# Performance work log

Measured on AMD Instinct MI355X. Metric: run time of the kernel, lower is better.

Reference implementation:

```python
import jax, jax.numpy as jnp
import numpy as np

CUTOFF = 0.32178
SCALE = 2.0 * 28.0 * CUTOFF


def setup_inputs() -> dict:
    rng = np.random.default_rng(0)
    N, E0, K = 20000, 160000, 9
    pos_np = rng.uniform(0.0, 28.0, (N, 2)).astype(np.float32)
    s = rng.integers(0, N, E0)
    d = rng.integers(0, N, E0)
    keep = s != d
    ei = np.stack([s[keep], d[keep]])
    ei = np.concatenate([ei, ei[::-1]], axis=1)
    ei = np.unique(ei.T, axis=0).T.astype(np.int64)  # symmetric, deduped, no self-loops

    def ncut(ei_, pos_):
        r, c = ei_
        w = np.linalg.norm(pos_[r] - pos_[c], axis=1)
        deg = np.bincount(r, minlength=pos_.shape[0]).astype(np.float64)
        deg[deg == 0] = 1.0
        return w * (1.0 / deg[r] + 1.0 / deg[c])

    def graclus(ei_, w, n):
        # greedy heavy-weight matching in node-index order (graclus-style)
        o = np.argsort(ei_[0], kind='stable')
        r, c, ww = ei_[0][o], ei_[1][o], w[o]
        ptr = np.searchsorted(r, np.arange(n + 1))
        cl = -np.ones(n, dtype=np.int64)
        cid = 0
        for i in range(n):
            if cl[i] >= 0:
                continue
            best, bw = -1, -1.0
            for k in range(ptr[i], ptr[i + 1]):
                j = c[k]
                if cl[j] < 0 and j != i and ww[k] > bw:
                    bw, best = ww[k], j
            cl[i] = cid
            if best >= 0:
                cl[best] = cid
            cid += 1
        return cl, cid

    def pool_edges(ei_, cl):
        m = cl[ei_]
        m = m[:, m[0] != m[1]]
        return np.unique(m.T, axis=0).T

    def seg_mean(v, cl, c):
        out = np.zeros((c, v.shape[1]), dtype=np.float64)
        np.add.at(out, cl, v)
        cnt = np.bincount(cl, minlength=c).astype(np.float64)
        return (out / cnt[:, None]).astype(np.float32)

    cl1, C1 = graclus(ei, ncut(ei, pos_np), N)
    ei2 = pool_edges(ei, cl1)
    pos2 = seg_mean(pos_np, cl1, C1)
    cl2, C2 = graclus(ei2, ncut(ei2, pos2), C1)
    ei3 = pool_edges(ei2, cl2)

    def prm(*shape):
        return jnp.asarray(rng.normal(0.0, 0.1, shape).astype(np.float32))

    def sig(k):
        return jnp.asarray(rng.uniform(0.5, 1.5, (k, 2)).astype(np.float32))

    return {
        'x': jnp.asarray(rng.standard_normal((N, 1)).astype(np.float32)),
        'pos': jnp.asarray(pos_np),
        'edge_index1': jnp.asarray(ei, dtype=jnp.int32),
        'cluster1': jnp.asarray(cl1, dtype=jnp.int32),
        'edge_index2': jnp.asarray(ei2, dtype=jnp.int32),
        'cluster2': jnp.asarray(cl2, dtype=jnp.int32),
        'edge_index3': jnp.asarray(ei3, dtype=jnp.int32),
        'batch': jnp.zeros((C2,), dtype=jnp.int32),
        'g1': prm(1, K, 32), 'mu1': prm(K, 2) + 0.5, 'sigma1': sig(K), 'root1': prm(1, 32), 'b1': prm(32),
        'g2': prm(32, K, 64), 'mu2': prm(K, 2) + 0.5, 'sigma2': sig(K), 'root2': prm(32, 64), 'b2': prm(64),
        'g3': prm(64, K, 64), 'mu3': prm(K, 2) + 0.5, 'sigma3': sig(K), 'root3': prm(64, 64), 'b3': prm(64),
        'fw': prm(64, 128), 'fb': prm(128),
    }


def _pseudo(pos, ei):
    # edge pseudo-coordinates: (pos[col]-pos[row]) / (2*28*cutoff) + 0.5
    return (pos[ei[1]] - pos[ei[0]]) / SCALE + 0.5


def _gmm_conv(x, ei, ea, g, mu, sigma, root, bias, n):
    # GMMConv: mean over neighbors of sum_k gauss_k(e_ij) * (x_j @ G_k), plus root weight and bias
    row, col = ei[0], ei[1]
    d = ea[:, None, :] - mu[None]                                       # [E,K,2]
    w = jnp.exp(-0.5 * jnp.sum(d * d / (sigma[None] ** 2), axis=-1))    # [E,K]
    msg = jnp.einsum('ei,iko,ek->eo', x[row], g, w)                     # [E,out]
    agg = jax.ops.segment_sum(msg, col, num_segments=n)
    cnt = jax.ops.segment_sum(jnp.ones_like(col, dtype=x.dtype), col, num_segments=n)
    return agg / jnp.maximum(cnt, 1.0)[:, None] + x @ root + bias


def _seg_mean(v, seg, n):
    s = jax.ops.segment_sum(v, seg, num_segments=n)
    c = jax.ops.segment_sum(jnp.ones((v.shape[0],), v.dtype), seg, num_segments=n)
    return s / jnp.maximum(c, 1.0)[:, None]


def _forward(x, pos, edge_index1, cluster1, edge_index2, cluster2, edge_index3, batch,
             g1, mu1, sigma1, root1, b1, g2, mu2, sigma2, root2, b2,
             g3, mu3, sigma3, root3, b3, fw, fb):
    N = x.shape[0]
    C1 = cluster2.shape[0]
    C2 = batch.shape[0]
    h = jax.nn.elu(_gmm_conv(x, edge_index1, _pseudo(pos, edge_index1), g1, mu1, sigma1, root1, b1, N))
    h = jax.ops.segment_max(h, cluster1, num_segments=C1)               # max_pool x
    pos2 = _seg_mean(pos, cluster1, C1)                                  # max_pool pos (mean)
    h = jax.nn.elu(_gmm_conv(h, edge_index2, _pseudo(pos2, edge_index2), g2, mu2, sigma2, root2, b2, C1))
    h = jax.ops.segment_max(h, cluster2, num_segments=C2)
    pos3 = _seg_mean(pos2, cluster2, C2)
    h = jax.nn.elu(_gmm_conv(h, edge_index3, _pseudo(pos3, edge_index3), g3, mu3, sigma3, root3, b3, C2))
    gm = _seg_mean(h, batch, 1)                                          # global_mean_pool (1 graph)
    return gm @ fw + fb                                                  # forward returns fc1(x)


def reference(x, pos, edge_index1, cluster1, edge_index2, cluster2, edge_index3, batch,
              g1, mu1, sigma1, root1, b1, g2, mu2, sigma2, root2, b2,
              g3, mu3, sigma3, root3, b3, fw, fb):
    return _forward(x, pos, edge_index1, cluster1, edge_index2, cluster2, edge_index3, batch,
                    g1, mu1, sigma1, root1, b1, g2, mu2, sigma2, root2, b2,
                    g3, mu3, sigma3, root3, b3, fw, fb)
```

## Files before the change

kernel.cpp:

```cpp
#include <hip/hip_runtime.h>
#include <math.h>

static constexpr float SCALE_F = (float)(2.0 * 28.0 * 0.32178);

__device__ __forceinline__ unsigned mapf(float f){
    unsigned u = __float_as_uint(f);
    return (u & 0x80000000u) ? ~u : (u | 0x80000000u);
}
__device__ __forceinline__ float unmapf(unsigned m){
    unsigned u = (m & 0x80000000u) ? (m ^ 0x80000000u) : ~m;
    return __uint_as_float(u);
}
__device__ __forceinline__ float eluf(float x){ return x > 0.f ? x : expm1f(x); }

__global__ void init_all(unsigned* __restrict__ hmax, int nmax, float* __restrict__ zreg, int nz){
    int i = blockIdx.x*blockDim.x + threadIdx.x;
    int s = gridDim.x*blockDim.x;
    for (int k = i; k < nmax; k += s) hmax[k] = 0x007FFFFFu;
    for (int k = i; k < nz;   k += s) zreg[k] = 0.f;
}

__global__ void build_rowptr_all(const int* __restrict__ r1, int E1, int N1, int* __restrict__ rp1,
                                 const int* __restrict__ r2, int E2, int N2, int* __restrict__ rp2,
                                 const int* __restrict__ r3, int E3, int N3, int* __restrict__ rp3){
    int i = blockIdx.x*blockDim.x + threadIdx.x;
    const int* rows; int E; int n; int* rp;
    if (i <= N1)               { rows=r1; E=E1; n=i;            rp=rp1+n; }
    else if (i <= N1+1+N2)     { rows=r2; E=E2; n=i-(N1+1);     rp=rp2+n; }
    else if (i <= N1+N2+2+N3)  { rows=r3; E=E3; n=i-(N1+N2+2);  rp=rp3+n; }
    else return;
    int lo = 0, hi = E;
    while (lo < hi){ int mid = (lo+hi) >> 1; if (rows[mid] < n) lo = mid+1; else hi = mid; }
    *rp = lo;
}

__global__ __launch_bounds__(256) void l1_kernel(const float* __restrict__ x, const float* __restrict__ pos,
    const int* __restrict__ ei1, int E1, const int* __restrict__ rp1, const int* __restrict__ cl1,
    const float* __restrict__ g1, const float* __restrict__ mu1, const float* __restrict__ sg1,
    const float* __restrict__ rt1, const float* __restrict__ b1,
    unsigned* __restrict__ h2m, float* __restrict__ pos2s, float* __restrict__ cntc1, int N)
{
    int wv = threadIdx.x >> 6, lane = threadIdx.x & 63;
    int n = blockIdx.x*4 + wv;
    if (n >= N) return;
    const int* cols = ei1 + E1;
    float mx[9], my[9], ivx[9], ivy[9];
    #pragma unroll
    for (int k = 0; k < 9; k++){
        mx[k] = mu1[2*k]; my[k] = mu1[2*k+1];
        float sx = sg1[2*k], sy = sg1[2*k+1];
        ivx[k] = 1.f/(sx*sx); ivy[k] = 1.f/(sy*sy);
    }
    float px = pos[2*n], py = pos[2*n+1];
    int e0 = rp1[n], e1 = rp1[n+1];
    float s[9] = {0.f,0.f,0.f,0.f,0.f,0.f,0.f,0.f,0.f};
    for (int e = e0 + lane; e < e1; e += 64){
        int j = cols[e];
        float ux = (px - pos[2*j])/SCALE_F + 0.5f;
        float uy = (py - pos[2*j+1])/SCALE_F + 0.5f;
        float xj = x[j];
        #pragma unroll
        for (int k = 0; k < 9; k++){
            float dx = ux - mx[k], dy = uy - my[k];
            s[k] += xj * expf(-0.5f*(dx*dx*ivx[k] + dy*dy*ivy[k]));
        }
    }
    #pragma unroll
    for (int off = 32; off > 0; off >>= 1){
        #pragma unroll
        for (int k = 0; k < 9; k++) s[k] += __shfl_xor(s[k], off, 64);
    }
    float inv = 1.f / (float)max(e1 - e0, 1);
    int c = cl1[n];
    if (lane < 32){
        int o = lane;
        float acc = 0.f;
        #pragma unroll
        for (int k = 0; k < 9; k++) acc += g1[k*32+o] * s[k];
        float v = acc*inv + x[n]*rt1[o] + b1[o];
        atomicMax(&h2m[(size_t)c*32 + o], mapf(eluf(v)));
    }
    if (lane == 0){
        atomicAdd(&pos2s[2*c],   px);
        atomicAdd(&pos2s[2*c+1], py);
        atomicAdd(&cntc1[c], 1.f);
    }
}

__global__ __launch_bounds__(256) void l2_kernel(const unsigned* __restrict__ h2m,
    const float* __restrict__ pos2s, const float* __restrict__ cntc1,
    const int* __restrict__ ei2, int E2, const int* __restrict__ rp2, const int* __restrict__ cl2,
    const float* __restrict__ g2, const float* __restrict__ mu2, const float* __restrict__ sg2,
    const float* __restrict__ rt2, const float* __restrict__ b2,
    unsigned* __restrict__ h3m, float* __restrict__ pos3s, float* __restrict__ cntc2)
{
    int n = blockIdx.x, t = threadIdx.x;
    __shared__ float mus[18], ivs[18];
    __shared__ int   jc[64];
    __shared__ float Wc[64*9];
    __shared__ float Sp[8*288];
    __shared__ float Ssum[288];
    __shared__ float xn_s[32];
    __shared__ float red1[4*64], red2[4*64];
    if (t < 9){
        mus[2*t] = mu2[2*t]; mus[2*t+1] = mu2[2*t+1];
        float sx = sg2[2*t], sy = sg2[2*t+1];
        ivs[2*t] = 1.f/(sx*sx); ivs[2*t+1] = 1.f/(sy*sy);
    }
    if (t < 32) xn_s[t] = unmapf(h2m[(size_t)n*32 + t]);
    int e0 = rp2[n], e1 = rp2[n+1], deg = e1 - e0;
    float cn = fmaxf(cntc1[n], 1.f);
    float px = pos2s[2*n]/cn, py = pos2s[2*n+1]/cn;
    const int* cols = ei2 + E2;
    int i = t & 31, g = t >> 5;
    float sacc[9] = {0.f,0.f,0.f,0.f,0.f,0.f,0.f,0.f,0.f};
    __syncthreads();
    for (int base = e0; base < e1; base += 64){
        int ne = min(64, e1 - base);
        if (t < ne){
            int j = cols[base + t];
            jc[t] = j;
            float cj = fmaxf(cntc1[j], 1.f);
            float ux = (px - pos2s[2*j]/cj)/SCALE_F + 0.5f;
            float uy = (py - pos2s[2*j+1]/cj)/SCALE_F + 0.5f;
            #pragma unroll
            for (int k = 0; k < 9; k++){
                float dx = ux - mus[2*k], dy = uy - mus[2*k+1];
                Wc[t*9+k] = expf(-0.5f*(dx*dx*ivs[2*k] + dy*dy*ivs[2*k+1]));
            }
        }
        __syncthreads();
        for (int jj = g; jj < ne; jj += 8){
            int j = jc[jj];
            float xji = unmapf(h2m[(size_t)j*32 + i]);
            #pragma unroll
            for (int k = 0; k < 9; k++) sacc[k] += xji * Wc[jj*9 + k];
        }
        __syncthreads();
    }
    #pragma unroll
    for (int k = 0; k < 9; k++) Sp[g*288 + i*9 + k] = sacc[k];
    __syncthreads();
    for (int idx = t; idx < 288; idx += 256){
        float v = 0.f;
        #pragma unroll
        for (int gg = 0; gg < 8; gg++) v += Sp[gg*288 + idx];
        Ssum[idx] = v;
    }
    __syncthreads();
    int o = t & 63, p = t >> 6;
    float acc = 0.f;
    for (int idx = p*72; idx < p*72 + 72; idx++) acc += g2[idx*64 + o] * Ssum[idx];
    float racc = 0.f;
    #pragma unroll
    for (int ii = p*8; ii < p*8 + 8; ii++) racc += xn_s[ii] * rt2[ii*64 + o];
    red1[p*64+o] = acc; red2[p*64+o] = racc;
    __syncthreads();
    if (t < 64){
        float agg = red1[t] + red1[64+t] + red1[128+t] + red1[192+t];
        float rr  = red2[t] + red2[64+t] + red2[128+t] + red2[192+t];
        float inv = 1.f / (float)max(deg, 1);
        float h = eluf(agg*inv + rr + b2[t]);
        int c = cl2[n];
        atomicMax(&h3m[(size_t)c*64 + t], mapf(h));
        if (t == 0){
            atomicAdd(&pos3s[2*c],   px);
            atomicAdd(&pos3s[2*c+1], py);
            atomicAdd(&cntc2[c], 1.f);
        }
    }
}

__global__ __launch_bounds__(256) void l3_kernel(const unsigned* __restrict__ h3m,
    const float* __restrict__ pos3s, const float* __restrict__ cntc2,
    const int* __restrict__ ei3, int E3, const int* __restrict__ rp3,
    const float* __restrict__ g3, const float* __restrict__ mu3, const float* __restrict__ sg3,
    const float* __restrict__ rt3, const float* __restrict__ b3,
    float* __restrict__ gpart)
{
    int n = blockIdx.x, t = threadIdx.x;
    __shared__ float mus[18], ivs[18];
    __shared__ int   jc[64];
    __shared__ float Wc[64*9];
    __shared__ float Sp[4*576];
    __shared__ float Ssum[576];
    __shared__ float xn_s[64];
    __shared__ float red1[4*64], red2[4*64];
    if (t < 9){
        mus[2*t] = mu3[2*t]; mus[2*t+1] = mu3[2*t+1];
        float sx = sg3[2*t], sy = sg3[2*t+1];
        ivs[2*t] = 1.f/(sx*sx); ivs[2*t+1] = 1.f/(sy*sy);
    }
    if (t < 64) xn_s[t] = unmapf(h3m[(size_t)n*64 + t]);
    int e0 = rp3[n], e1 = rp3[n+1], deg = e1 - e0;
    float cn = fmaxf(cntc2[n], 1.f);
    float px = pos3s[2*n]/cn, py = pos3s[2*n+1]/cn;
    const int* cols = ei3 + E3;
    int i = t & 63, wv = t >> 6;
    float sacc[9] = {0.f,0.f,0.f,0.f,0.f,0.f,0.f,0.f,0.f};
    __syncthreads();
    for (int base = e0; base < e1; base += 64){
        int ne = min(64, e1 - base);
        if (t < ne){
            int j = cols[base + t];
            jc[t] = j;
            float cj = fmaxf(cntc2[j], 1.f);
            float ux = (px - pos3s[2*j]/cj)/SCALE_F + 0.5f;
            float uy = (py - pos3s[2*j+1]/cj)/SCALE_F + 0.5f;
            #pragma unroll
            for (int k = 0; k < 9; k++){
                float dx = ux - mus[2*k], dy = uy - mus[2*k+1];
                Wc[t*9+k] = expf(-0.5f*(dx*dx*ivs[2*k] + dy*dy*ivs[2*k+1]));
            }
        }
        __syncthreads();
        for (int jj = wv; jj < ne; jj += 4){
            int j = jc[jj];
            float xji = unmapf(h3m[(size_t)j*64 + i]);
            #pragma unroll
            for (int k = 0; k < 9; k++) sacc[k] += xji * Wc[jj*9 + k];
        }
        __syncthreads();
    }
    #pragma unroll
    for (int k = 0; k < 9; k++) Sp[wv*576 + i*9 + k] = sacc[k];
    __syncthreads();
    for (int idx = t; idx < 576; idx += 256){
        float v = Sp[idx] + Sp[576 + idx] + Sp[1152 + idx] + Sp[1728 + idx];
        Ssum[idx] = v;
    }
    __syncthreads();
    int o = t & 63, p = t >> 6;
    float acc = 0.f;
    for (int idx = p*144; idx < p*144 + 144; idx++) acc += g3[idx*64 + o] * Ssum[idx];
    float racc = 0.f;
    #pragma unroll
    for (int ii = p*16; ii < p*16 + 16; ii++) racc += xn_s[ii] * rt3[ii*64 + o];
    red1[p*64+o] = acc; red2[p*64+o] = racc;
    __syncthreads();
    if (t < 64){
        float agg = red1[t] + red1[64+t] + red1[128+t] + red1[192+t];
        float rr  = red2[t] + red2[64+t] + red2[128+t] + red2[192+t];
        float inv = 1.f / (float)max(deg, 1);
        float h = eluf(agg*inv + rr + b3[t]);
        atomicAdd(&gpart[(size_t)(n & 63)*64 + t], h);
    }
}

__global__ void final_kernel(const float* __restrict__ gpart, const float* __restrict__ fw,
                             const float* __restrict__ fb, float* __restrict__ out, int C2){
    __shared__ float gs[64];
    __shared__ float red[2*64];
    int t = threadIdx.x;
    int o = t & 63, h = t >> 6;
    float a = 0.f;
    for (int p = h*32; p < h*32 + 32; p++) a += gpart[p*64 + o];
    red[h*64 + o] = a;
    __syncthreads();
    if (t < 64) gs[t] = (red[t] + red[64+t]) / (float)C2;
    __syncthreads();
    float acc = fb[t];
    for (int o2 = 0; o2 < 64; o2++) acc += gs[o2] * fw[o2*128 + t];
    out[t] = acc;
}

extern "C" void kernel_launch(void* const* d_in, const int* in_sizes, int n_in,
                              void* d_out, int out_size, void* d_ws, size_t ws_size,
                              hipStream_t stream)
{
    const float* x    = (const float*)d_in[0];
    const float* pos  = (const float*)d_in[1];
    const int*   ei1  = (const int*)d_in[2];
    const int*   cl1  = (const int*)d_in[3];
    const int*   ei2  = (const int*)d_in[4];
    const int*   cl2  = (const int*)d_in[5];
    const int*   ei3  = (const int*)d_in[6];
    const float* g1   = (const float*)d_in[8];
    const float* mu1  = (const float*)d_in[9];
    const float* sg1  = (const float*)d_in[10];
    const float* rt1  = (const float*)d_in[11];
    const float* b1   = (const float*)d_in[12];
    const float* g2   = (const float*)d_in[13];
    const float* mu2  = (const float*)d_in[14];
    const float* sg2  = (const float*)d_in[15];
    const float* rt2  = (const float*)d_in[16];
    const float* b2   = (const float*)d_in[17];
    const float* g3   = (const float*)d_in[18];
    const float* mu3  = (const float*)d_in[19];
    const float* sg3  = (const float*)d_in[20];
    const float* rt3  = (const float*)d_in[21];
    const float* b3   = (const float*)d_in[22];
    const float* fw   = (const float*)d_in[23];
    const float* fb   = (const float*)d_in[24];
    float* out = (float*)d_out;

    const int N  = in_sizes[0];
    const int E1 = in_sizes[2] / 2;
    const int C1 = in_sizes[5];
    const int E2 = in_sizes[4] / 2;
    const int C2 = in_sizes[7];
    const int E3 = in_sizes[6] / 2;

    float* w = (float*)d_ws;
    size_t off = 0;
    int* rp1 = (int*)(w + off); off += (size_t)N + 1;
    int* rp2 = (int*)(w + off); off += (size_t)C1 + 1;
    int* rp3 = (int*)(w + off); off += (size_t)C2 + 1;
    unsigned* h2m = (unsigned*)(w + off); off += (size_t)C1 * 32;
    unsigned* h3m = (unsigned*)(w + off); off += (size_t)C2 * 64;
    float* pos2s = w + off; off += (size_t)2 * C1;
    float* cntc1 = w + off; off += (size_t)C1;
    float* pos3s = w + off; off += (size_t)2 * C2;
    float* cntc2 = w + off; off += (size_t)C2;
    float* gpart = w + off; off += 64*64;

    const int nmax = C1*32 + C2*64;
    const int nz   = 3*C1 + 3*C2 + 64*64;
    init_all<<<dim3(256), dim3(256), 0, stream>>>(h2m, nmax, pos2s, nz);

    int nrp = N + C1 + C2 + 3;
    build_rowptr_all<<<dim3((nrp + 255)/256), dim3(256), 0, stream>>>(
        ei1, E1, N, rp1, ei2, E2, C1, rp2, ei3, E3, C2, rp3);

    l1_kernel<<<dim3((N + 3)/4), dim3(256), 0, stream>>>(x, pos, ei1, E1, rp1, cl1,
        g1, mu1, sg1, rt1, b1, h2m, pos2s, cntc1, N);
    l2_kernel<<<dim3(C1), dim3(256), 0, stream>>>(h2m, pos2s, cntc1, ei2, E2, rp2, cl2,
        g2, mu2, sg2, rt2, b2, h3m, pos3s, cntc2);
    l3_kernel<<<dim3(C2), dim3(256), 0, stream>>>(h3m, pos3s, cntc2, ei3, E3, rp3,
        g3, mu3, sg3, rt3, b3, gpart);
    final_kernel<<<dim3(1), dim3(128), 0, stream>>>(gpart, fw, fb, out, C2);
}
```

Baseline: 246.1 us.

## Remap GMM conv layers to wave-per-node and merge prep kernels

```diff
diff --git a/kernel.cpp b/kernel.cpp
--- a/kernel.cpp
+++ b/kernel.cpp
@@ -13,35 +13,45 @@
 }
 __device__ __forceinline__ float eluf(float x){ return x > 0.f ? x : expm1f(x); }
 
-__global__ void init_all(unsigned* __restrict__ hmax, int nmax, float* __restrict__ zreg, int nz){
-    int i = blockIdx.x*blockDim.x + threadIdx.x;
-    int s = gridDim.x*blockDim.x;
-    for (int k = i; k < nmax; k += s) hmax[k] = 0x007FFFFFu;
-    for (int k = i; k < nz;   k += s) zreg[k] = 0.f;
-}
-
-__global__ void build_rowptr_all(const int* __restrict__ r1, int E1, int N1, int* __restrict__ rp1,
-                                 const int* __restrict__ r2, int E2, int N2, int* __restrict__ rp2,
-                                 const int* __restrict__ r3, int E3, int N3, int* __restrict__ rp3){
-    int i = blockIdx.x*blockDim.x + threadIdx.x;
-    const int* rows; int E; int n; int* rp;
-    if (i <= N1)               { rows=r1; E=E1; n=i;            rp=rp1+n; }
-    else if (i <= N1+1+N2)     { rows=r2; E=E2; n=i-(N1+1);     rp=rp2+n; }
-    else if (i <= N1+N2+2+N3)  { rows=r3; E=E3; n=i-(N1+N2+2);  rp=rp3+n; }
-    else return;
-    int lo = 0, hi = E;
-    while (lo < hi){ int mid = (lo+hi) >> 1; if (rows[mid] < n) lo = mid+1; else hi = mid; }
-    *rp = lo;
-}
-
-__global__ __launch_bounds__(256) void l1_kernel(const float* __restrict__ x, const float* __restrict__ pos,
+__device__ __forceinline__ void wave_sync(){
+    __builtin_amdgcn_wave_barrier();
+    asm volatile("s_waitcnt lgkmcnt(0)" ::: "memory");
+    __builtin_amdgcn_wave_barrier();
+}
+
+__global__ void prep_kernel(const float* __restrict__ x, const float* __restrict__ pos, int N,
+    const int* __restrict__ ei1, int E1, const int* __restrict__ ei2, int E2, int C1,
+    const int* __restrict__ ei3, int E3, int C2,
+    int* __restrict__ rp1, int* __restrict__ rp2, int* __restrict__ rp3,
+    unsigned* __restrict__ hmax, int nmax, float* __restrict__ zreg, int nz,
+    float4* __restrict__ xp1)
+{
+    int i0 = blockIdx.x*blockDim.x + threadIdx.x, gs = gridDim.x*blockDim.x;
+    for (int i = i0; i < nmax; i += gs) hmax[i] = 0x007FFFFFu;
+    for (int i = i0; i < nz;   i += gs) zreg[i] = 0.f;
+    for (int i = i0; i < N;    i += gs) xp1[i] = make_float4(pos[2*i], pos[2*i+1], x[i], 0.f);
+    int nrp = N + C1 + C2 + 3;
+    for (int i = i0; i < nrp; i += gs){
+        const int* rows; int E, n; int* rp;
+        if (i <= N)            { rows = ei1; E = E1; n = i;            rp = rp1 + n; }
+        else if (i <= N+1+C1)  { rows = ei2; E = E2; n = i - (N+1);    rp = rp2 + n; }
+        else                   { rows = ei3; E = E3; n = i - (N+C1+2); rp = rp3 + n; }
+        int lo = 0, hi = E;
+        while (lo < hi){ int m = (lo+hi) >> 1; if (rows[m] < n) lo = m+1; else hi = m; }
+        *rp = lo;
+    }
+}
+
+__global__ __launch_bounds__(256) void l1_kernel(const float4* __restrict__ xp1,
     const int* __restrict__ ei1, int E1, const int* __restrict__ rp1, const int* __restrict__ cl1,
     const float* __restrict__ g1, const float* __restrict__ mu1, const float* __restrict__ sg1,
     const float* __restrict__ rt1, const float* __restrict__ b1,
-    unsigned* __restrict__ h2m, float* __restrict__ pos2s, float* __restrict__ cntc1, int N)
-{
-    int wv = threadIdx.x >> 6, lane = threadIdx.x & 63;
-    int n = blockIdx.x*4 + wv;
+    unsigned* __restrict__ h2m, float4* __restrict__ pos2s4, int N)
+{
+    int t = threadIdx.x;
+    int lane = t & 63, wv = t >> 6;
+    int q = lane >> 4, il = lane & 15;
+    int n = (blockIdx.x*4 + wv)*4 + q;
     if (n >= N) return;
     const int* cols = ei1 + E1;
     float mx[9], my[9], ivx[9], ivy[9];
@@ -51,200 +61,183 @@
         float sx = sg1[2*k], sy = sg1[2*k+1];
         ivx[k] = 1.f/(sx*sx); ivy[k] = 1.f/(sy*sy);
     }
-    float px = pos[2*n], py = pos[2*n+1];
+    float4 me = xp1[n];
+    float px = me.x, py = me.y, xn = me.z;
     int e0 = rp1[n], e1 = rp1[n+1];
     float s[9] = {0.f,0.f,0.f,0.f,0.f,0.f,0.f,0.f,0.f};
-    for (int e = e0 + lane; e < e1; e += 64){
+    for (int e = e0 + il; e < e1; e += 16){
         int j = cols[e];
-        float ux = (px - pos[2*j])/SCALE_F + 0.5f;
-        float uy = (py - pos[2*j+1])/SCALE_F + 0.5f;
-        float xj = x[j];
+        float4 pj = xp1[j];
+        float ux = (px - pj.x)/SCALE_F + 0.5f;
+        float uy = (py - pj.y)/SCALE_F + 0.5f;
         #pragma unroll
         for (int k = 0; k < 9; k++){
             float dx = ux - mx[k], dy = uy - my[k];
-            s[k] += xj * expf(-0.5f*(dx*dx*ivx[k] + dy*dy*ivy[k]));
-        }
-    }
-    #pragma unroll
-    for (int off = 32; off > 0; off >>= 1){
+            s[k] += pj.z * expf(-0.5f*(dx*dx*ivx[k] + dy*dy*ivy[k]));
+        }
+    }
+    #pragma unroll
+    for (int off = 8; off > 0; off >>= 1){
         #pragma unroll
-        for (int k = 0; k < 9; k++) s[k] += __shfl_xor(s[k], off, 64);
+        for (int k = 0; k < 9; k++) s[k] += __shfl_xor(s[k], off, 16);
     }
     float inv = 1.f / (float)max(e1 - e0, 1);
     int c = cl1[n];
-    if (lane < 32){
-        int o = lane;
+    #pragma unroll
+    for (int oo = 0; oo < 2; oo++){
+        int o = il + oo*16;
         float acc = 0.f;
         #pragma unroll
         for (int k = 0; k < 9; k++) acc += g1[k*32+o] * s[k];
-        float v = acc*inv + x[n]*rt1[o] + b1[o];
+        float v = acc*inv + xn*rt1[o] + b1[o];
         atomicMax(&h2m[(size_t)c*32 + o], mapf(eluf(v)));
     }
-    if (lane == 0){
-        atomicAdd(&pos2s[2*c],   px);
-        atomicAdd(&pos2s[2*c+1], py);
-        atomicAdd(&cntc1[c], 1.f);
+    if (il == 0){
+        atomicAdd(&pos2s4[c].x, px);
+        atomicAdd(&pos2s4[c].y, py);
+        atomicAdd(&pos2s4[c].z, 1.f);
     }
 }
 
 __global__ __launch_bounds__(256) void l2_kernel(const unsigned* __restrict__ h2m,
-    const float* __restrict__ pos2s, const float* __restrict__ cntc1,
+    const float4* __restrict__ pos2s4,
     const int* __restrict__ ei2, int E2, const int* __restrict__ rp2, const int* __restrict__ cl2,
     const float* __restrict__ g2, const float* __restrict__ mu2, const float* __restrict__ sg2,
     const float* __restrict__ rt2, const float* __restrict__ b2,
-    unsigned* __restrict__ h3m, float* __restrict__ pos3s, float* __restrict__ cntc2)
-{
-    int n = blockIdx.x, t = threadIdx.x;
-    __shared__ float mus[18], ivs[18];
-    __shared__ int   jc[64];
-    __shared__ float Wc[64*9];
-    __shared__ float Sp[8*288];
-    __shared__ float Ssum[288];
-    __shared__ float xn_s[32];
-    __shared__ float red1[4*64], red2[4*64];
-    if (t < 9){
-        mus[2*t] = mu2[2*t]; mus[2*t+1] = mu2[2*t+1];
-        float sx = sg2[2*t], sy = sg2[2*t+1];
-        ivs[2*t] = 1.f/(sx*sx); ivs[2*t+1] = 1.f/(sy*sy);
-    }
-    if (t < 32) xn_s[t] = unmapf(h2m[(size_t)n*32 + t]);
+    unsigned* __restrict__ h3m, float4* __restrict__ pos3s4, int C1)
+{
+    __shared__ float wbuf[4][576];
+    __shared__ int   jcs[4][64];
+    __shared__ float xns[4][32];
+    int t = threadIdx.x, l = t & 63, w = t >> 6;
+    int n = blockIdx.x*4 + w;
+    if (n >= C1) return;
+    const int* cols = ei2 + E2;
+    float mx[9], my[9], ivx[9], ivy[9];
+    #pragma unroll
+    for (int k = 0; k < 9; k++){
+        mx[k] = mu2[2*k]; my[k] = mu2[2*k+1];
+        float sx = sg2[2*k], sy = sg2[2*k+1];
+        ivx[k] = 1.f/(sx*sx); ivy[k] = 1.f/(sy*sy);
+    }
+    if (l < 32) xns[w][l] = unmapf(h2m[(size_t)n*32 + l]);
+    float4 pm = pos2s4[n];
+    float cn = fmaxf(pm.z, 1.f);
+    float px = pm.x/cn, py = pm.y/cn;
     int e0 = rp2[n], e1 = rp2[n+1], deg = e1 - e0;
-    float cn = fmaxf(cntc1[n], 1.f);
-    float px = pos2s[2*n]/cn, py = pos2s[2*n+1]/cn;
-    const int* cols = ei2 + E2;
-    int i = t & 31, g = t >> 5;
+    int i = l & 31, half = l >> 5;
     float sacc[9] = {0.f,0.f,0.f,0.f,0.f,0.f,0.f,0.f,0.f};
-    __syncthreads();
     for (int base = e0; base < e1; base += 64){
         int ne = min(64, e1 - base);
-        if (t < ne){
-            int j = cols[base + t];
-            jc[t] = j;
-            float cj = fmaxf(cntc1[j], 1.f);
-            float ux = (px - pos2s[2*j]/cj)/SCALE_F + 0.5f;
-            float uy = (py - pos2s[2*j+1]/cj)/SCALE_F + 0.5f;
+        if (l < ne){
+            int j = cols[base + l];
+            jcs[w][l] = j;
+            float4 pj = pos2s4[j];
+            float cj = fmaxf(pj.z, 1.f);
+            float ux = (px - pj.x/cj)/SCALE_F + 0.5f;
+            float uy = (py - pj.y/cj)/SCALE_F + 0.5f;
             #pragma unroll
             for (int k = 0; k < 9; k++){
-                float dx = ux - mus[2*k], dy = uy - mus[2*k+1];
-                Wc[t*9+k] = expf(-0.5f*(dx*dx*ivs[2*k] + dy*dy*ivs[2*k+1]));
+                float dx = ux - mx[k], dy = uy - my[k];
+                wbuf[w][l*9+k] = expf(-0.5f*(dx*dx*ivx[k] + dy*dy*ivy[k]));
             }
         }
-        __syncthreads();
-        for (int jj = g; jj < ne; jj += 8){
-            int j = jc[jj];
+        wave_sync();
+        for (int jj = half; jj < ne; jj += 2){
+            int j = jcs[w][jj];
             float xji = unmapf(h2m[(size_t)j*32 + i]);
             #pragma unroll
-            for (int k = 0; k < 9; k++) sacc[k] += xji * Wc[jj*9 + k];
-        }
-        __syncthreads();
-    }
-    #pragma unroll
-    for (int k = 0; k < 9; k++) Sp[g*288 + i*9 + k] = sacc[k];
-    __syncthreads();
-    for (int idx = t; idx < 288; idx += 256){
-        float v = 0.f;
+            for (int k = 0; k < 9; k++) sacc[k] += xji * wbuf[w][jj*9+k];
+        }
+        wave_sync();
+    }
+    #pragma unroll
+    for (int k = 0; k < 9; k++) sacc[k] += __shfl_xor(sacc[k], 32, 64);
+    if (l < 32){
         #pragma unroll
-        for (int gg = 0; gg < 8; gg++) v += Sp[gg*288 + idx];
-        Ssum[idx] = v;
-    }
-    __syncthreads();
-    int o = t & 63, p = t >> 6;
+        for (int k = 0; k < 9; k++) wbuf[w][l*9+k] = sacc[k];
+    }
+    wave_sync();
     float acc = 0.f;
-    for (int idx = p*72; idx < p*72 + 72; idx++) acc += g2[idx*64 + o] * Ssum[idx];
+    #pragma unroll 8
+    for (int idx = 0; idx < 288; idx++) acc += g2[idx*64 + l] * wbuf[w][idx];
     float racc = 0.f;
-    #pragma unroll
-    for (int ii = p*8; ii < p*8 + 8; ii++) racc += xn_s[ii] * rt2[ii*64 + o];
-    red1[p*64+o] = acc; red2[p*64+o] = racc;
-    __syncthreads();
-    if (t < 64){
-        float agg = red1[t] + red1[64+t] + red1[128+t] + red1[192+t];
-        float rr  = red2[t] + red2[64+t] + red2[128+t] + red2[192+t];
-        float inv = 1.f / (float)max(deg, 1);
-        float h = eluf(agg*inv + rr + b2[t]);
-        int c = cl2[n];
-        atomicMax(&h3m[(size_t)c*64 + t], mapf(h));
-        if (t == 0){
-            atomicAdd(&pos3s[2*c],   px);
-            atomicAdd(&pos3s[2*c+1], py);
-            atomicAdd(&cntc2[c], 1.f);
-        }
+    #pragma unroll 8
+    for (int ii = 0; ii < 32; ii++) racc += xns[w][ii] * rt2[ii*64 + l];
+    float inv = 1.f / (float)max(deg, 1);
+    float h = eluf(acc*inv + racc + b2[l]);
+    int c = cl2[n];
+    atomicMax(&h3m[(size_t)c*64 + l], mapf(h));
+    if (l == 0){
+        atomicAdd(&pos3s4[c].x, px);
+        atomicAdd(&pos3s4[c].y, py);
+        atomicAdd(&pos3s4[c].z, 1.f);
     }
 }
 
 __global__ __launch_bounds__(256) void l3_kernel(const unsigned* __restrict__ h3m,
-    const float* __restrict__ pos3s, const float* __restrict__ cntc2,
+    const float4* __restrict__ pos3s4,
     const int* __restrict__ ei3, int E3, const int* __restrict__ rp3,
     const float* __restrict__ g3, const float* __restrict__ mu3, const float* __restrict__ sg3,
     const float* __restrict__ rt3, const float* __restrict__ b3,
-    float* __restrict__ gpart)
-{
-    int n = blockIdx.x, t = threadIdx.x;
-    __shared__ float mus[18], ivs[18];
-    __shared__ int   jc[64];
-    __shared__ float Wc[64*9];
-    __shared__ float Sp[4*576];
-    __shared__ float Ssum[576];
-    __shared__ float xn_s[64];
-    __shared__ float red1[4*64], red2[4*64];
-    if (t < 9){
-        mus[2*t] = mu3[2*t]; mus[2*t+1] = mu3[2*t+1];
-        float sx = sg3[2*t], sy = sg3[2*t+1];
-        ivs[2*t] = 1.f/(sx*sx); ivs[2*t+1] = 1.f/(sy*sy);
-    }
-    if (t < 64) xn_s[t] = unmapf(h3m[(size_t)n*64 + t]);
+    float* __restrict__ gpart, int C2)
+{
+    __shared__ float wbuf[4][576];
+    __shared__ int   jcs[4][64];
+    __shared__ float xns[4][64];
+    int t = threadIdx.x, l = t & 63, w = t >> 6;
+    int n = blockIdx.x*4 + w;
+    if (n >= C2) return;
+    const int* cols = ei3 + E3;
+    float mx[9], my[9], ivx[9], ivy[9];
+    #pragma unroll
+    for (int k = 0; k < 9; k++){
+        mx[k] = mu3[2*k]; my[k] = mu3[2*k+1];
+        float sx = sg3[2*k], sy = sg3[2*k+1];
+        ivx[k] = 1.f/(sx*sx); ivy[k] = 1.f/(sy*sy);
+    }
+    xns[w][l] = unmapf(h3m[(size_t)n*64 + l]);
+    float4 pm = pos3s4[n];
+    float cn = fmaxf(pm.z, 1.f);
+    float px = pm.x/cn, py = pm.y/cn;
     int e0 = rp3[n], e1 = rp3[n+1], deg = e1 - e0;
-    float cn = fmaxf(cntc2[n], 1.f);
-    float px = pos3s[2*n]/cn, py = pos3s[2*n+1]/cn;
-    const int* cols = ei3 + E3;
-    int i = t & 63, wv = t >> 6;
     float sacc[9] = {0.f,0.f,0.f,0.f,0.f,0.f,0.f,0.f,0.f};
-    __syncthreads();
     for (int base = e0; base < e1; base += 64){
         int ne = min(64, e1 - base);
-        if (t < ne){
-            int j = cols[base + t];
-            jc[t] = j;
-            float cj = fmaxf(cntc2[j], 1.f);
-            float ux = (px - pos3s[2*j]/cj)/SCALE_F + 0.5f;
-            float uy = (py - pos3s[2*j+1]/cj)/SCALE_F + 0.5f;
+        if (l < ne){
+            int j = cols[base + l];
+            jcs[w][l] = j;
+            float4 pj = pos3s4[j];
+            float cj = fmaxf(pj.z, 1.f);
+            float ux = (px - pj.x/cj)/SCALE_F + 0.5f;
+            float uy = (py - pj.y/cj)/SCALE_F + 0.5f;
             #pragma unroll
             for (int k = 0; k < 9; k++){
-                float dx = ux - mus[2*k], dy = uy - mus[2*k+1];
-                Wc[t*9+k] = expf(-0.5f*(dx*dx*ivs[2*k] + dy*dy*ivs[2*k+1]));
+                float dx = ux - mx[k], dy = uy - my[k];
+                wbuf[w][l*9+k] = expf(-0.5f*(dx*dx*ivx[k] + dy*dy*ivy[k]));
             }
         }
-        __syncthreads();
-        for (int jj = wv; jj < ne; jj += 4){
-            int j = jc[jj];
-            float xji = unmapf(h3m[(size_t)j*64 + i]);
+        wave_sync();
+        for (int jj = 0; jj < ne; jj++){
+            int j = jcs[w][jj];
+            float xji = unmapf(h3m[(size_t)j*64 + l]);
             #pragma unroll
-            for (int k = 0; k < 9; k++) sacc[k] += xji * Wc[jj*9 + k];
-        }
-        __syncthreads();
-    }
-    #pragma unroll
-    for (int k = 0; k < 9; k++) Sp[wv*576 + i*9 + k] = sacc[k];
-    __syncthreads();
-    for (int idx = t; idx < 576; idx += 256){
-        float v = Sp[idx] + Sp[576 + idx] + Sp[1152 + idx] + Sp[1728 + idx];
-        Ssum[idx] = v;
-    }
-    __syncthreads();
-    int o = t & 63, p = t >> 6;
+            for (int k = 0; k < 9; k++) sacc[k] += xji * wbuf[w][jj*9+k];
+        }
+        wave_sync();
+    }
+    #pragma unroll
+    for (int k = 0; k < 9; k++) wbuf[w][l*9+k] = sacc[k];
+    wave_sync();
     float acc = 0.f;
-    for (int idx = p*144; idx < p*144 + 144; idx++) acc += g3[idx*64 + o] * Ssum[idx];
+    #pragma unroll 8
+    for (int idx = 0; idx < 576; idx++) acc += g3[idx*64 + l] * wbuf[w][idx];
     float racc = 0.f;
-    #pragma unroll
-    for (int ii = p*16; ii < p*16 + 16; ii++) racc += xn_s[ii] * rt3[ii*64 + o];
-    red1[p*64+o] = acc; red2[p*64+o] = racc;
-    __syncthreads();
-    if (t < 64){
-        float agg = red1[t] + red1[64+t] + red1[128+t] + red1[192+t];
-        float rr  = red2[t] + red2[64+t] + red2[128+t] + red2[192+t];
-        float inv = 1.f / (float)max(deg, 1);
-        float h = eluf(agg*inv + rr + b3[t]);
-        atomicAdd(&gpart[(size_t)(n & 63)*64 + t], h);
-    }
+    #pragma unroll 8
+    for (int ii = 0; ii < 64; ii++) racc += xns[w][ii] * rt3[ii*64 + l];
+    float inv = 1.f / (float)max(deg, 1);
+    float h = eluf(acc*inv + racc + b3[l]);
+    atomicAdd(&gpart[(size_t)(n & 63)*64 + l], h);
 }
 
 __global__ void final_kernel(const float* __restrict__ gpart, const float* __restrict__ fw,
@@ -303,30 +296,27 @@
 
     float* w = (float*)d_ws;
     size_t off = 0;
+    float4* xp1    = (float4*)(w + off); off += (size_t)4*N;
+    float4* pos2s4 = (float4*)(w + off); off += (size_t)4*C1;
+    float4* pos3s4 = (float4*)(w + off); off += (size_t)4*C2;
+    float*  gpart  = w + off;            off += 64*64;
     int* rp1 = (int*)(w + off); off += (size_t)N + 1;
     int* rp2 = (int*)(w + off); off += (size_t)C1 + 1;
     int* rp3 = (int*)(w + off); off += (size_t)C2 + 1;
     unsigned* h2m = (unsigned*)(w + off); off += (size_t)C1 * 32;
     unsigned* h3m = (unsigned*)(w + off); off += (size_t)C2 * 64;
-    float* pos2s = w + off; off += (size_t)2 * C1;
-    float* cntc1 = w + off; off += (size_t)C1;
-    float* pos3s = w + off; off += (size_t)2 * C2;
-    float* cntc2 = w + off; off += (size_t)C2;
-    float* gpart = w + off; off += 64*64;
 
     const int nmax = C1*32 + C2*64;
-    const int nz   = 3*C1 + 3*C2 + 64*64;
-    init_all<<<dim3(256), dim3(256), 0, stream>>>(h2m, nmax, pos2s, nz);
-
-    int nrp = N + C1 + C2 + 3;
-    build_rowptr_all<<<dim3((nrp + 255)/256), dim3(256), 0, stream>>>(
-        ei1, E1, N, rp1, ei2, E2, C1, rp2, ei3, E3, C2, rp3);
-
-    l1_kernel<<<dim3((N + 3)/4), dim3(256), 0, stream>>>(x, pos, ei1, E1, rp1, cl1,
-        g1, mu1, sg1, rt1, b1, h2m, pos2s, cntc1, N);
-    l2_kernel<<<dim3(C1), dim3(256), 0, stream>>>(h2m, pos2s, cntc1, ei2, E2, rp2, cl2,
-        g2, mu2, sg2, rt2, b2, h3m, pos3s, cntc2);
-    l3_kernel<<<dim3(C2), dim3(256), 0, stream>>>(h3m, pos3s, cntc2, ei3, E3, rp3,
-        g3, mu3, sg3, rt3, b3, gpart);
+    const int nz   = 4*C1 + 4*C2 + 64*64;
+    prep_kernel<<<dim3(1024), dim3(256), 0, stream>>>(x, pos, N,
+        ei1, E1, ei2, E2, C1, ei3, E3, C2,
+        rp1, rp2, rp3, h2m, nmax, (float*)pos2s4, nz, xp1);
+
+    l1_kernel<<<dim3((N + 15)/16), dim3(256), 0, stream>>>(xp1, ei1, E1, rp1, cl1,
+        g1, mu1, sg1, rt1, b1, h2m, pos2s4, N);
+    l2_kernel<<<dim3((C1 + 3)/4), dim3(256), 0, stream>>>(h2m, pos2s4, ei2, E2, rp2, cl2,
+        g2, mu2, sg2, rt2, b2, h3m, pos3s4, C1);
+    l3_kernel<<<dim3((C2 + 3)/4), dim3(256), 0, stream>>>(h3m, pos3s4, ei3, E3, rp3,
+        g3, mu3, sg3, rt3, b3, gpart, C2);
     final_kernel<<<dim3(1), dim3(128), 0, stream>>>(gpart, fw, fb, out, C2);
 }
```

Result: faster. 229.2 us (-6.9%).
